# Kernel tuning notes

Measured on AMD Instinct MI355X. Metric: run time of the kernel, lower is better.

## Reference

```python
import jax, jax.numpy as jnp
import numpy as np

B, L, D, H = 2, 256, 512, 8
DH = D // H
EPS = 1e-12
NEG = -1000000000000000.0


def setup_inputs() -> dict:
    key = jax.random.key(0)
    ks = jax.random.split(key, 16)
    s = 0.02
    return {
        "inputs": jax.random.normal(ks[0], (B, L, D), jnp.float32),
        "pos_embedding": jax.random.normal(ks[1], (B, L, L, D), jnp.float32),
        "seq_mask": jnp.ones((B, L), jnp.int32),
        "Wq": jax.random.normal(ks[2], (D, D), jnp.float32) * s,
        "bq": jnp.zeros((D,), jnp.float32),
        "Wk": jax.random.normal(ks[3], (D, D), jnp.float32) * s,
        "bk": jnp.zeros((D,), jnp.float32),
        "Wv": jax.random.normal(ks[4], (D, D), jnp.float32) * s,
        "bv": jnp.zeros((D,), jnp.float32),
        "Wr": jax.random.normal(ks[5], (D, D), jnp.float32) * s,
        "br": jnp.zeros((D,), jnp.float32),
        "u": jax.random.normal(ks[6], (H, DH), jnp.float32),
        "v": jax.random.normal(ks[7], (H, DH), jnp.float32),
        "Wf": jax.random.normal(ks[8], (D, D), jnp.float32) * s,
        "bf": jnp.zeros((D,), jnp.float32),
        "gamma": jnp.ones((D,), jnp.float32),
        "beta": jnp.zeros((D,), jnp.float32),
    }


def _layer_norm(x, gamma, beta, eps):
    mu = jnp.mean(x, axis=-1, keepdims=True)
    var = jnp.mean(jnp.square(x - mu), axis=-1, keepdims=True)
    return (x - mu) * jax.lax.rsqrt(var + eps) * gamma + beta


def reference(inputs, pos_embedding, seq_mask, Wq, bq, Wk, bk, Wv, bv, Wr, br,
              u, v, Wf, bf, gamma, beta):
    b, l, d = inputs.shape
    # projections (nn.Linear: x @ W.T + b)
    q = (inputs @ Wq.T + bq).reshape(b, l, H, DH).transpose(0, 2, 1, 3)  # [B,H,L,DH]
    k = (inputs @ Wk.T + bk).reshape(b, l, H, DH).transpose(0, 2, 1, 3)
    vv = (inputs @ Wv.T + bv).reshape(b, l, H, DH).transpose(0, 2, 1, 3)
    rel = (pos_embedding @ Wr.T + br).reshape(b, l, l, H, DH)            # [B,L,L,H,DH]

    # A + C: content-content + content-bias
    A_C = jnp.einsum('bhid,bhjd->bhij', q + u[None, :, None, :], k)
    # B + D: position term against per-(i,j) relative embeddings
    B_D = jnp.einsum('bhid,bijhd->bhij', q + v[None, :, None, :], rel)

    score = (A_C + B_D) / np.sqrt(DH).astype(np.float32)
    invalid = (seq_mask == 0)[:, None, None, :]   # mask keys where seq_mask==0
    score = jnp.where(invalid, NEG, score)
    attn = jax.nn.softmax(score, axis=-1)

    ctx = jnp.einsum('bhij,bhjd->bhid', attn, vv)
    ctx = ctx.transpose(0, 2, 1, 3).reshape(b, l, d)

    # FFN (single dense) + residual + LayerNorm
    h = ctx @ Wf.T + bf
    return _layer_norm(h + inputs, gamma, beta, EPS)
```

## Files before the change

### kernel.cpp

```cpp
#include <hip/hip_runtime.h>
#include <cmath>

typedef __bf16 bf16x8 __attribute__((ext_vector_type(8)));
typedef float f32x4 __attribute__((ext_vector_type(4)));

__device__ __forceinline__ float4 ld4(const float* p) { return *reinterpret_cast<const float4*>(p); }
__device__ __forceinline__ void st4(float* p, float4 v) { *reinterpret_cast<float4*>(p) = v; }
__device__ __forceinline__ void fma4(float4& a, float s, const float4& v) {
    a.x = fmaf(s, v.x, a.x); a.y = fmaf(s, v.y, a.y);
    a.z = fmaf(s, v.z, a.z); a.w = fmaf(s, v.w, a.w);
}
__device__ __forceinline__ float dot4(const float4& a, const float4& b) {
    return a.x*b.x + a.y*b.y + a.z*b.z + a.w*b.w;
}
__device__ __forceinline__ unsigned short f2bf(float f) {
    unsigned int x = __float_as_uint(f);
    unsigned int r = x + 0x7FFFu + ((x >> 16) & 1u);
    return (unsigned short)(r >> 16);
}
__device__ __forceinline__ bf16x8 cvt8(float4 a, float4 b) {
    bf16x8 r;
    r[0] = (__bf16)a.x; r[1] = (__bf16)a.y; r[2] = (__bf16)a.z; r[3] = (__bf16)a.w;
    r[4] = (__bf16)b.x; r[5] = (__bf16)b.y; r[6] = (__bf16)b.z; r[7] = (__bf16)b.w;
    return r;
}

__device__ __forceinline__ void mfma_tile(
        const float* __restrict__ Abase, int ldA,
        const float* __restrict__ Bbase, int ldB,
        int K, int lane, f32x4 acc[4]) {
    int koff = (lane >> 4) * 8;
    int rr = lane & 15;
    const float* ap = Abase + rr * ldA + koff;
    const float* bp = Bbase + rr * ldB + koff;
#pragma unroll 2
    for (int k0 = 0; k0 < K; k0 += 32) {
        float4 a0  = ld4(ap + k0),            a1  = ld4(ap + k0 + 4);
        float4 b00 = ld4(bp + k0),            b01 = ld4(bp + k0 + 4);
        float4 b10 = ld4(bp + 16*ldB + k0),   b11 = ld4(bp + 16*ldB + k0 + 4);
        float4 b20 = ld4(bp + 32*ldB + k0),   b21 = ld4(bp + 32*ldB + k0 + 4);
        float4 b30 = ld4(bp + 48*ldB + k0),   b31 = ld4(bp + 48*ldB + k0 + 4);
        bf16x8 af = cvt8(a0, a1);
        acc[0] = __builtin_amdgcn_mfma_f32_16x16x32_bf16(af, cvt8(b00, b01), acc[0], 0, 0, 0);
        acc[1] = __builtin_amdgcn_mfma_f32_16x16x32_bf16(af, cvt8(b10, b11), acc[1], 0, 0, 0);
        acc[2] = __builtin_amdgcn_mfma_f32_16x16x32_bf16(af, cvt8(b20, b21), acc[2], 0, 0, 0);
        acc[3] = __builtin_amdgcn_mfma_f32_16x16x32_bf16(af, cvt8(b30, b31), acc[3], 0, 0, 0);
    }
}

__global__ __launch_bounds__(256) void k_wrt(
        const float* __restrict__ Wr, float* __restrict__ Wrt) {
    __shared__ float tile[32][33];
    int n0 = blockIdx.x * 32, k0 = blockIdx.y * 32;
    int tx = threadIdx.x & 31, ty = threadIdx.x >> 5;
#pragma unroll
    for (int r = 0; r < 4; r++) {
        int row = ty * 4 + r;
        tile[row][tx] = Wr[(n0 + row) * 512 + k0 + tx];
    }
    __syncthreads();
#pragma unroll
    for (int r = 0; r < 4; r++) {
        int row = ty * 4 + r;
        Wrt[(k0 + row) * 512 + n0 + tx] = tile[tx][row];
    }
}

__global__ __launch_bounds__(256) void k_qkv(
        const float* __restrict__ x,
        const float* __restrict__ Wq, const float* __restrict__ Wk, const float* __restrict__ Wv,
        const float* __restrict__ bq, const float* __restrict__ bk, const float* __restrict__ bv,
        float* __restrict__ qw, float* __restrict__ kw, float* __restrict__ vw) {
    int mat = blockIdx.z;
    const float* W   = (mat == 0) ? Wq : (mat == 1) ? Wk : Wv;
    const float* bias= (mat == 0) ? bq : (mat == 1) ? bk : bv;
    float* out       = (mat == 0) ? qw : (mat == 1) ? kw : vw;
    int m0 = blockIdx.x * 64, n0 = blockIdx.y * 64;
    int t = threadIdx.x, wv = t >> 6, lane = t & 63;
    f32x4 acc[4] = {{0,0,0,0},{0,0,0,0},{0,0,0,0},{0,0,0,0}};
    mfma_tile(x + (m0 + wv * 16) * 512, 512, W + n0 * 512, 512, 512, lane, acc);
    int h = n0 >> 6;
    int col = lane & 15, rbase = (lane >> 4) * 4;
#pragma unroll
    for (int c = 0; c < 4; c++) {
        int d = c * 16 + col;
        float bv_ = bias[n0 + d];
#pragma unroll
        for (int r = 0; r < 4; r++) {
            int m = m0 + wv * 16 + rbase + r;
            int b = m >> 8, i = m & 255;
            out[((b * 8 + h) * 256 + i) * 64 + d] = acc[c][r] + bv_;
        }
    }
}

__global__ __launch_bounds__(256) void k_small(
        const float* __restrict__ qw, const float* __restrict__ kw,
        const float* __restrict__ wrt,
        const float* __restrict__ u, const float* __restrict__ vb,
        const float* __restrict__ br,
        float* __restrict__ c_ws, float* __restrict__ uk_ws, float* __restrict__ vwr_ws) {
    int g = blockIdx.x * 256 + threadIdx.x;
    if (g < 4096) {
        int h = (g >> 8) & 7;
        const float* qrow = qw + g * 64;
        const float* brh = br + h * 64;
        const float* vbh = vb + h * 64;
        float s = 0.f;
#pragma unroll
        for (int d = 0; d < 64; d += 4) {
            float4 q4 = ld4(qrow + d), b4 = ld4(brh + d), v4 = ld4(vbh + d);
            s += (q4.x + v4.x) * b4.x + (q4.y + v4.y) * b4.y
               + (q4.z + v4.z) * b4.z + (q4.w + v4.w) * b4.w;
        }
        c_ws[g] = s;
    } else if (g < 8192) {
        int g2 = g - 4096;
        int h = (g2 >> 8) & 7;
        const float* krow = kw + g2 * 64;
        const float* uh = u + h * 64;
        float s = 0.f;
#pragma unroll
        for (int d = 0; d < 64; d += 4) s += dot4(ld4(krow + d), ld4(uh + d));
        uk_ws[g2] = s;
    } else if (g < 12288) {
        int g3 = g - 8192;
        int h = g3 >> 9, e = g3 & 511;
        const float* wr_row = wrt + e * 512 + h * 64;
        const float* vbh = vb + h * 64;
        float s = 0.f;
#pragma unroll
        for (int d = 0; d < 64; d += 4) s += dot4(ld4(wr_row + d), ld4(vbh + d));
        vwr_ws[h * 512 + e] = s;
    }
}

__global__ __launch_bounds__(256) void k_w(
        const float* __restrict__ qw, const float* __restrict__ wrt,
        const float* __restrict__ vwr_ws, float* __restrict__ w_ws) {
    int h = blockIdx.z;
    int m0 = blockIdx.x * 64, n0 = blockIdx.y * 64;
    int t = threadIdx.x, wv = t >> 6, lane = t & 63;
    int b = m0 >> 8, i0 = m0 & 255;
    f32x4 acc[4] = {{0,0,0,0},{0,0,0,0},{0,0,0,0},{0,0,0,0}};
    mfma_tile(qw + ((b * 8 + h) * 256 + i0 + wv * 16) * 64, 64,
              wrt + n0 * 512 + h * 64, 512, 64, lane, acc);
    int col = lane & 15, rbase = (lane >> 4) * 4;
#pragma unroll
    for (int c = 0; c < 4; c++) {
        int n = n0 + c * 16 + col;
        float vw_ = vwr_ws[h * 512 + n];
#pragma unroll
        for (int r = 0; r < 4; r++) {
            int m = m0 + wv * 16 + rbase + r;
            w_ws[((size_t)m * 8 + h) * 512 + n] = acc[c][r] + vw_;
        }
    }
}

__global__ __launch_bounds__(256) void k_ac(
        const float* __restrict__ qw, const float* __restrict__ kw,
        const float* __restrict__ uk_ws, const float* __restrict__ c_ws,
        float* __restrict__ ac_ws) {
    int bh = blockIdx.z;
    int b = bh >> 3, h = bh & 7;
    int i0 = blockIdx.x * 64, j0 = blockIdx.y * 64;
    int t = threadIdx.x, wv = t >> 6, lane = t & 63;
    f32x4 acc[4] = {{0,0,0,0},{0,0,0,0},{0,0,0,0},{0,0,0,0}};
    mfma_tile(qw + ((b * 8 + h) * 256 + i0 + wv * 16) * 64, 64,
              kw + ((b * 8 + h) * 256 + j0) * 64, 64, 64, lane, acc);
    int col = lane & 15, rbase = (lane >> 4) * 4;
#pragma unroll
    for (int c = 0; c < 4; c++) {
        int j = j0 + c * 16 + col;
        float ukv = uk_ws[(b * 8 + h) * 256 + j];
#pragma unroll
        for (int r = 0; r < 4; r++) {
            int i = i0 + wv * 16 + rbase + r;
            ac_ws[((b * 256 + i) * 8 + h) * 256 + j] = acc[c][r] + ukv + c_ws[(b * 8 + h) * 256 + i];
        }
    }
}

__global__ __launch_bounds__(512, 4) void k_attn(
        const float* __restrict__ pos, const float* __restrict__ w_ws,
        const float* __restrict__ ac_ws, const float* __restrict__ vw,
        const int* __restrict__ seq_mask, float* __restrict__ ctx) {
    int bi = blockIdx.x;
    int b = bi >> 8, i = bi & 255;
    int t = threadIdx.x;
    int wv = t >> 6, lane = t & 63;
    __shared__ float sc[8][260];
    __shared__ float4 part[8][4][16];
    __shared__ unsigned short wl[8 * 520];

    {
        int h = t >> 6;
        int e0 = (t & 63) * 8;
        const float* src = w_ws + ((size_t)bi * 8 + h) * 512 + e0;
        float4 a = ld4(src);
        float4 c = ld4(src + 4);
        ushort4 u0, u1;
        u0.x = f2bf(a.x); u0.y = f2bf(a.y); u0.z = f2bf(a.z); u0.w = f2bf(a.w);
        u1.x = f2bf(c.x); u1.y = f2bf(c.y); u1.z = f2bf(c.z); u1.w = f2bf(c.w);
        *reinterpret_cast<ushort4*>(&wl[h * 520 + e0]) = u0;
        *reinterpret_cast<ushort4*>(&wl[h * 520 + e0 + 4]) = u1;
    }
    __syncthreads();

    const bf16x8* wfb = reinterpret_cast<const bf16x8*>(&wl[(lane & 7) * 520 + (lane >> 4) * 8]);

    const float* pbase = pos + (size_t)bi * (256 * 512);
    int arow = lane & 15;
    int eoff = (lane >> 4) * 8;
    const float* pr0 = pbase + (size_t)((wv * 2 + 0) * 16 + arow) * 512 + eoff;
    const float* pr1 = pbase + (size_t)((wv * 2 + 1) * 16 + arow) * 512 + eoff;
    f32x4 acc0 = {0, 0, 0, 0}, acc1 = {0, 0, 0, 0};
    for (int e = 0; e < 16; e += 2) {
        float4 a00 = ld4(pr0 + e * 32), a01 = ld4(pr0 + e * 32 + 4);
        float4 a10 = ld4(pr1 + e * 32), a11 = ld4(pr1 + e * 32 + 4);
        float4 b00 = ld4(pr0 + e * 32 + 32), b01 = ld4(pr0 + e * 32 + 36);
        float4 b10 = ld4(pr1 + e * 32 + 32), b11 = ld4(pr1 + e * 32 + 36);
        bf16x8 Bf0 = wfb[e * 4];
        bf16x8 Bf1 = wfb[e * 4 + 4];
        acc0 = __builtin_amdgcn_mfma_f32_16x16x32_bf16(cvt8(a00, a01), Bf0, acc0, 0, 0, 0);
        acc1 = __builtin_amdgcn_mfma_f32_16x16x32_bf16(cvt8(a10, a11), Bf0, acc1, 0, 0, 0);
        acc0 = __builtin_amdgcn_mfma_f32_16x16x32_bf16(cvt8(b00, b01), Bf1, acc0, 0, 0, 0);
        acc1 = __builtin_amdgcn_mfma_f32_16x16x32_bf16(cvt8(b10, b11), Bf1, acc1, 0, 0, 0);
    }
    {
        int h = lane & 15;
        int rbase = (lane >> 4) * 4;
        if (h < 8) {
#pragma unroll
            for (int r = 0; r < 4; r++) {
                sc[h][(wv * 2 + 0) * 16 + rbase + r] = acc0[r];
                sc[h][(wv * 2 + 1) * 16 + rbase + r] = acc1[r];
            }
        }
    }
    __syncthreads();

    {
        int h = wv;
        const float* acrow = ac_ws + ((b * 256 + i) * 8 + h) * 256;
        float vals[4];
        float mx = -INFINITY;
#pragma unroll
        for (int r = 0; r < 4; r++) {
            int j = lane + r * 64;
            float s = (sc[h][j] + acrow[j]) * 0.125f;
            if (seq_mask[b * 256 + j] == 0) s = -1e15f;
            vals[r] = s;
            mx = fmaxf(mx, s);
        }
#pragma unroll
        for (int m = 32; m >= 1; m >>= 1) mx = fmaxf(mx, __shfl_xor(mx, m, 64));
        float sum = 0.f;
#pragma unroll
        for (int r = 0; r < 4; r++) { vals[r] = __expf(vals[r] - mx); sum += vals[r]; }
#pragma unroll
        for (int m = 32; m >= 1; m >>= 1) sum += __shfl_xor(sum, m, 64);
        float inv = 1.0f / sum;
#pragma unroll
        for (int r = 0; r < 4; r++) sc[h][lane + r * 64] = vals[r] * inv;
    }
    __syncthreads();

    {
        int h = wv;
        int d4 = (lane & 15) * 4;
        int js = lane >> 4;
        const float* vbase = vw + (size_t)(b * 8 + h) * 256 * 64;
        float4 acc = {0, 0, 0, 0};
        for (int r = 0; r < 64; r++) {
            int j = js * 64 + r;
            float p = sc[h][j];
            float4 v4 = ld4(&vbase[j * 64 + d4]);
            fma4(acc, p, v4);
        }
        part[h][js][lane & 15] = acc;
    }
    __syncthreads();
    {
        int h = wv;
        if ((lane >> 4) == 0) {
            int l = lane & 15;
            float4 a0 = part[h][0][l], a1 = part[h][1][l], a2 = part[h][2][l], a3 = part[h][3][l];
            float4 o;
            o.x = a0.x + a1.x + a2.x + a3.x;
            o.y = a0.y + a1.y + a2.y + a3.y;
            o.z = a0.z + a1.z + a2.z + a3.z;
            o.w = a0.w + a1.w + a2.w + a3.w;
            st4(ctx + (size_t)(b * 256 + i) * 512 + h * 64 + l * 4, o);
        }
    }
}

__global__ __launch_bounds__(256) void k_ffn(
        const float* __restrict__ A, const float* __restrict__ Wf,
        const float* __restrict__ bias, const float* __restrict__ resid,
        float* __restrict__ outp) {
    int m0 = blockIdx.x * 64, n0 = blockIdx.y * 64;
    int t = threadIdx.x, wv = t >> 6, lane = t & 63;
    f32x4 acc[4] = {{0,0,0,0},{0,0,0,0},{0,0,0,0},{0,0,0,0}};
    mfma_tile(A + (m0 + wv * 16) * 512, 512, Wf + n0 * 512, 512, 512, lane, acc);
    int col = lane & 15, rbase = (lane >> 4) * 4;
#pragma unroll
    for (int c = 0; c < 4; c++) {
        int n = n0 + c * 16 + col;
        float bv_ = bias[n];
#pragma unroll
        for (int r = 0; r < 4; r++) {
            int m = m0 + wv * 16 + rbase + r;
            outp[m * 512 + n] = acc[c][r] + bv_ + resid[m * 512 + n];
        }
    }
}

__global__ __launch_bounds__(256) void k_ln(
        const float* __restrict__ tmp, const float* __restrict__ gamma,
        const float* __restrict__ beta, float* __restrict__ out) {
    int m = blockIdx.x, t = threadIdx.x;
    int wv = t >> 6, lane = t & 63;
    float2 xv = *reinterpret_cast<const float2*>(&tmp[m * 512 + t * 2]);
    __shared__ float red[4];
    float s = xv.x + xv.y;
#pragma unroll
    for (int k = 32; k >= 1; k >>= 1) s += __shfl_xor(s, k, 64);
    if (lane == 0) red[wv] = s;
    __syncthreads();
    float mu = (red[0] + red[1] + red[2] + red[3]) * (1.0f / 512.0f);
    __syncthreads();
    float dx = xv.x - mu, dy = xv.y - mu;
    float vs = dx * dx + dy * dy;
#pragma unroll
    for (int k = 32; k >= 1; k >>= 1) vs += __shfl_xor(vs, k, 64);
    if (lane == 0) red[wv] = vs;
    __syncthreads();
    float var = (red[0] + red[1] + red[2] + red[3]) * (1.0f / 512.0f);
    float rstd = rsqrtf(var + 1e-12f);
    float2 g = *reinterpret_cast<const float2*>(&gamma[t * 2]);
    float2 be = *reinterpret_cast<const float2*>(&beta[t * 2]);
    float2 o;
    o.x = dx * rstd * g.x + be.x;
    o.y = dy * rstd * g.y + be.y;
    *reinterpret_cast<float2*>(&out[m * 512 + t * 2]) = o;
}

extern "C" void kernel_launch(void* const* d_in, const int* in_sizes, int n_in,
                              void* d_out, int out_size, void* d_ws, size_t ws_size,
                              hipStream_t stream) {
    const float* x     = (const float*)d_in[0];
    const float* pos   = (const float*)d_in[1];
    const int*   smask = (const int*)d_in[2];
    const float* Wq = (const float*)d_in[3];
    const float* bq = (const float*)d_in[4];
    const float* Wk = (const float*)d_in[5];
    const float* bk = (const float*)d_in[6];
    const float* Wv = (const float*)d_in[7];
    const float* bv = (const float*)d_in[8];
    const float* Wr = (const float*)d_in[9];
    const float* br = (const float*)d_in[10];
    const float* u  = (const float*)d_in[11];
    const float* vb = (const float*)d_in[12];
    const float* Wf = (const float*)d_in[13];
    const float* bf = (const float*)d_in[14];
    const float* gamma = (const float*)d_in[15];
    const float* beta  = (const float*)d_in[16];
    float* out = (float*)d_out;

    float* ws = (float*)d_ws;
    float* q_ws   = ws;
    float* k_ws   = q_ws  + 262144;
    float* v_ws   = k_ws  + 262144;
    float* w_ws   = v_ws  + 262144;
    float* c_ws   = w_ws  + 2097152;
    float* uk_ws  = c_ws  + 4096;
    float* vwr_ws = uk_ws + 4096;
    float* ac_ws  = vwr_ws + 4096;
    float* ctx_ws = ac_ws + 1048576;
    float* tmp_ws = ctx_ws + 262144;
    float* wrt_ws = tmp_ws + 262144;

    k_wrt<<<dim3(16, 16), 256, 0, stream>>>(Wr, wrt_ws);
    k_qkv<<<dim3(8, 8, 3), 256, 0, stream>>>(x, Wq, Wk, Wv, bq, bk, bv, q_ws, k_ws, v_ws);
    k_small<<<dim3(48), 256, 0, stream>>>(q_ws, k_ws, wrt_ws, u, vb, br, c_ws, uk_ws, vwr_ws);
    k_w<<<dim3(8, 8, 8), 256, 0, stream>>>(q_ws, wrt_ws, vwr_ws, w_ws);
    k_ac<<<dim3(4, 4, 16), 256, 0, stream>>>(q_ws, k_ws, uk_ws, c_ws, ac_ws);
    k_attn<<<dim3(512), 512, 0, stream>>>(pos, w_ws, ac_ws, v_ws, smask, ctx_ws);
    k_ffn<<<dim3(8, 8), 256, 0, stream>>>(ctx_ws, Wf, bf, x, tmp_ws);
    k_ln<<<dim3(512), 256, 0, stream>>>(tmp_ws, gamma, beta, out);
}
```

Measured before the change: 119.3 us.

## Stage coalesced pos-embedding rows through LDS as bf16 before MFMA

The attention kernel's pos-embedding GEMV now has each wave load whole 1 KB row segments with fully coalesced float4 loads, 16 rows in flight per lane. It converts them to bf16 into a per-wave LDS staging buffer and feeds the MFMA from LDS instead of gathering strided 32-byte fragments straight from global memory. The partial-sum buffer reuses the staging memory, LDS padding is dropped, and two block barriers are removed where each wave only touches its own data. The aim is better streaming bandwidth on the dominant pos read. In exchange, block LDS grows to about 80 KB, which cuts resident blocks per CU, and there is an extra LDS round trip.

```diff
diff --git a/kernel.cpp b/kernel.cpp
--- a/kernel.cpp
+++ b/kernel.cpp
@@ -17,6 +17,11 @@
     unsigned int x = __float_as_uint(f);
     unsigned int r = x + 0x7FFFu + ((x >> 16) & 1u);
     return (unsigned short)(r >> 16);
+}
+__device__ __forceinline__ ushort4 cvt4u(float4 a) {
+    ushort4 u;
+    u.x = f2bf(a.x); u.y = f2bf(a.y); u.z = f2bf(a.z); u.w = f2bf(a.w);
+    return u;
 }
 __device__ __forceinline__ bf16x8 cvt8(float4 a, float4 b) {
     bf16x8 r;
@@ -190,9 +195,9 @@
     int b = bi >> 8, i = bi & 255;
     int t = threadIdx.x;
     int wv = t >> 6, lane = t & 63;
-    __shared__ float sc[8][260];
-    __shared__ float4 part[8][4][16];
-    __shared__ unsigned short wl[8 * 520];
+    __shared__ unsigned short wl[8 * 512];
+    __shared__ float sc[8][256];
+    __shared__ unsigned short stage[8][4096];
 
     {
         int h = t >> 6;
@@ -200,43 +205,42 @@
         const float* src = w_ws + ((size_t)bi * 8 + h) * 512 + e0;
         float4 a = ld4(src);
         float4 c = ld4(src + 4);
-        ushort4 u0, u1;
-        u0.x = f2bf(a.x); u0.y = f2bf(a.y); u0.z = f2bf(a.z); u0.w = f2bf(a.w);
-        u1.x = f2bf(c.x); u1.y = f2bf(c.y); u1.z = f2bf(c.z); u1.w = f2bf(c.w);
-        *reinterpret_cast<ushort4*>(&wl[h * 520 + e0]) = u0;
-        *reinterpret_cast<ushort4*>(&wl[h * 520 + e0 + 4]) = u1;
-    }
-    __syncthreads();
-
-    const bf16x8* wfb = reinterpret_cast<const bf16x8*>(&wl[(lane & 7) * 520 + (lane >> 4) * 8]);
-
-    const float* pbase = pos + (size_t)bi * (256 * 512);
+        *reinterpret_cast<ushort4*>(&wl[h * 512 + e0])     = cvt4u(a);
+        *reinterpret_cast<ushort4*>(&wl[h * 512 + e0 + 4]) = cvt4u(c);
+    }
+    __syncthreads();
+
+    const float* pb = pos + (size_t)bi * (256 * 512);
+    int jbase = wv * 32;
+    unsigned short* sb = &stage[wv][0];
     int arow = lane & 15;
-    int eoff = (lane >> 4) * 8;
-    const float* pr0 = pbase + (size_t)((wv * 2 + 0) * 16 + arow) * 512 + eoff;
-    const float* pr1 = pbase + (size_t)((wv * 2 + 1) * 16 + arow) * 512 + eoff;
-    f32x4 acc0 = {0, 0, 0, 0}, acc1 = {0, 0, 0, 0};
-    for (int e = 0; e < 16; e += 2) {
-        float4 a00 = ld4(pr0 + e * 32), a01 = ld4(pr0 + e * 32 + 4);
-        float4 a10 = ld4(pr1 + e * 32), a11 = ld4(pr1 + e * 32 + 4);
-        float4 b00 = ld4(pr0 + e * 32 + 32), b01 = ld4(pr0 + e * 32 + 36);
-        float4 b10 = ld4(pr1 + e * 32 + 32), b11 = ld4(pr1 + e * 32 + 36);
-        bf16x8 Bf0 = wfb[e * 4];
-        bf16x8 Bf1 = wfb[e * 4 + 4];
-        acc0 = __builtin_amdgcn_mfma_f32_16x16x32_bf16(cvt8(a00, a01), Bf0, acc0, 0, 0, 0);
-        acc1 = __builtin_amdgcn_mfma_f32_16x16x32_bf16(cvt8(a10, a11), Bf0, acc1, 0, 0, 0);
-        acc0 = __builtin_amdgcn_mfma_f32_16x16x32_bf16(cvt8(b00, b01), Bf1, acc0, 0, 0, 0);
-        acc1 = __builtin_amdgcn_mfma_f32_16x16x32_bf16(cvt8(b10, b11), Bf1, acc1, 0, 0, 0);
-    }
-    {
+    int koff = (lane >> 4) * 8;
+
+#pragma unroll
+    for (int jt = 0; jt < 2; jt++) {
+        f32x4 acc = {0, 0, 0, 0};
+#pragma unroll
+        for (int eh = 0; eh < 2; eh++) {
+            const float* src = pb + (size_t)(jbase + jt * 16) * 512 + eh * 256 + lane * 4;
+            float4 tmp[16];
+#pragma unroll
+            for (int s = 0; s < 16; s++) tmp[s] = ld4(src + s * 512);
+#pragma unroll
+            for (int s = 0; s < 16; s++) {
+                *reinterpret_cast<ushort4*>(&sb[s * 256 + lane * 4]) = cvt4u(tmp[s]);
+            }
+#pragma unroll
+            for (int es = 0; es < 8; es++) {
+                bf16x8 af = *reinterpret_cast<const bf16x8*>(&sb[arow * 256 + es * 32 + koff]);
+                bf16x8 bf = *reinterpret_cast<const bf16x8*>(&wl[(lane & 7) * 512 + (eh * 8 + es) * 32 + koff]);
+                acc = __builtin_amdgcn_mfma_f32_16x16x32_bf16(af, bf, acc, 0, 0, 0);
+            }
+        }
         int h = lane & 15;
         int rbase = (lane >> 4) * 4;
         if (h < 8) {
 #pragma unroll
-            for (int r = 0; r < 4; r++) {
-                sc[h][(wv * 2 + 0) * 16 + rbase + r] = acc0[r];
-                sc[h][(wv * 2 + 1) * 16 + rbase + r] = acc1[r];
-            }
+            for (int r = 0; r < 4; r++) sc[h][jbase + jt * 16 + rbase + r] = acc[r];
         }
     }
     __syncthreads();
@@ -265,8 +269,8 @@
 #pragma unroll
         for (int r = 0; r < 4; r++) sc[h][lane + r * 64] = vals[r] * inv;
     }
-    __syncthreads();
-
+
+    float4* part = reinterpret_cast<float4*>(&stage[0][0]);
     {
         int h = wv;
         int d4 = (lane & 15) * 4;
@@ -279,14 +283,14 @@
             float4 v4 = ld4(&vbase[j * 64 + d4]);
             fma4(acc, p, v4);
         }
-        part[h][js][lane & 15] = acc;
-    }
-    __syncthreads();
+        part[(h * 4 + js) * 16 + (lane & 15)] = acc;
+    }
     {
         int h = wv;
         if ((lane >> 4) == 0) {
             int l = lane & 15;
-            float4 a0 = part[h][0][l], a1 = part[h][1][l], a2 = part[h][2][l], a3 = part[h][3][l];
+            float4 a0 = part[(h * 4 + 0) * 16 + l], a1 = part[(h * 4 + 1) * 16 + l];
+            float4 a2 = part[(h * 4 + 2) * 16 + l], a3 = part[(h * 4 + 3) * 16 + l];
             float4 o;
             o.x = a0.x + a1.x + a2.x + a3.x;
             o.y = a0.y + a1.y + a2.y + a3.y;
```

Result: no change. 117.3 us (-1.7%).
